# Optimization experiments

Hardware: AMD Instinct MI355X
Metric: run time of the kernel (lower is better)

The kernel has to match this reference:

```python
import jax, jax.numpy as jnp
import numpy as np

P, B, S = 128, 32, 64          # num_packet, batch, bytes per packet
E = 50                          # byte/packet embedding size (hard-coded in module)
Hb = 128; Hp = 128; Po = 128   # byte hidden, packet hidden, packet output
V = 256 * 256; NCLS = 11


def setup_inputs() -> dict:
    key = jax.random.key(0)
    ks = jax.random.split(key, 12)
    rn = lambda k, shp, s: (jax.random.normal(k, shp, jnp.float32) * s)
    return {
        'flow': jax.random.randint(ks[0], (P, B, S), 0, V),
        'emb': rn(ks[1], (V, E), 0.1),
        'byte_Wih': rn(ks[2], (2, 3 * Hb, E), 1.0 / np.sqrt(E)),
        'byte_Whh': rn(ks[3], (2, 3 * Hb, Hb), 1.0 / np.sqrt(Hb)),
        'byte_attn_W': rn(ks[4], (E, 2 * Hb), 1.0 / np.sqrt(2 * Hb)),
        'byte_attn_b': jnp.zeros((E,), jnp.float32),
        'pkt_Wih': rn(ks[5], (2, 3 * Hp, E), 1.0 / np.sqrt(E)),
        'pkt_Whh': rn(ks[6], (2, 3 * Hp, Hp), 1.0 / np.sqrt(Hp)),
        'pkt_attn_W': rn(ks[7], (Po, 2 * Hp), 1.0 / np.sqrt(2 * Hp)),
        'pkt_attn_b': jnp.zeros((Po,), jnp.float32),
        'cls_W': rn(ks[8], (NCLS, Po), 1.0 / np.sqrt(Po)),
        'cls_b': jnp.zeros((NCLS,), jnp.float32),
        'h0_bytes': rn(ks[9], (P, 2, B, Hb), 1.0),   # per-packet random h0 (torch.randn in fwd)
        'h0_packet': rn(ks[10], (2, B, Hp), 1.0),
    }


def _gru_dir(xW, h0, Whh, H):
    # xW: (S, N, 3H) precomputed input projections; h0: (N, H). PyTorch gate order r,z,n; no bias.
    def step(h, xw):
        hW = h @ Whh.T
        r = jax.nn.sigmoid(xw[:, :H] + hW[:, :H])
        z = jax.nn.sigmoid(xw[:, H:2 * H] + hW[:, H:2 * H])
        n = jnp.tanh(xw[:, 2 * H:] + r * hW[:, 2 * H:])
        h_new = (1.0 - z) * n + z * h
        return h_new, h_new
    hT, ys = jax.lax.scan(step, h0, xW)
    return ys, hT


def bigru(x, h0, Wih, Whh, H):
    # x: (S, N, E); h0: (2, N, H) -> outputs (S, N, 2H), final hidden (2, N, H)
    xWf = jnp.einsum('sne,ge->sng', x, Wih[0])
    xWb = jnp.einsum('sne,ge->sng', x[::-1], Wih[1])
    yf, hf = _gru_dir(xWf, h0[0], Whh[0], H)
    yb, hb = _gru_dir(xWb, h0[1], Whh[1], H)
    return jnp.concatenate([yf, yb[::-1]], axis=-1), jnp.stack([hf, hb])


def reference(flow, emb, byte_Wih, byte_Whh, byte_attn_W, byte_attn_b,
              pkt_Wih, pkt_Whh, pkt_attn_W, pkt_attn_b, cls_W, cls_b,
              h0_bytes, h0_packet):
    Pn, Bn, Sn = flow.shape
    x = emb[flow]                                             # (P, B, S, E)
    # Fold packets into batch: one byte-level bi-GRU call instead of a Python loop over P.
    xs = x.transpose(2, 0, 1, 3).reshape(Sn, Pn * Bn, E)      # (S, P*B, E)
    h0b = h0_bytes.transpose(1, 0, 2, 3).reshape(2, Pn * Bn, Hb)
    y, hn = bigru(xs, h0b, byte_Wih, byte_Whh, Hb)            # y (S, P*B, 2Hb), hn (2, P*B, Hb)
    out = y.transpose(1, 0, 2).reshape(Pn, Bn, Sn, 2 * Hb)    # (P, B, S, 2Hb)
    # torch view(-1, 2Hb, 1) on each per-packet (2, B, Hb) final state == raw C-order reshape
    hn_p = hn.reshape(2, Pn, Bn, Hb).transpose(1, 0, 2, 3).reshape(Pn, Bn, 2 * Hb)
    aw = jax.nn.softmax(jnp.einsum('pbsh,pbh->pbs', out, hn_p), axis=-1)
    ctx = jnp.einsum('pbsh,pbs->pbh', out, aw)                # (P, B, 2Hb)
    enc = ctx @ byte_attn_W.T + byte_attn_b                   # (P, B, E)

    y2, hn2 = bigru(enc, h0_packet, pkt_Wih, pkt_Whh, Hp)     # (P, B, 2Hp), (2, B, Hp)
    out2 = y2.transpose(1, 0, 2)                              # (B, P, 2Hp)
    hn2v = hn2.reshape(Bn, 2 * Hp)                            # view(-1, byte_hidden*2) semantics
    aw2 = jax.nn.softmax(jnp.einsum('bph,bh->bp', out2, hn2v), axis=-1)
    ctx2 = jnp.einsum('bph,bp->bh', out2, aw2)                # (B, 2Hp)
    o = ctx2 @ pkt_attn_W.T + pkt_attn_b                      # (B, Po)
    return o @ cls_W.T + cls_b                                # (B, 11)
```

## Files before the change

### kernel.cpp

```cpp
#include <hip/hip_runtime.h>
#include <hip/hip_bf16.h>

#define PD 128
#define BD 32
#define SD 64
#define ED 50
#define HD 128
#define GD 384
#define ND 4096
#define VD 65536
#define LW 128

typedef __attribute__((ext_vector_type(8))) short bf16x8;
typedef __attribute__((ext_vector_type(4))) float f32x4;

__device__ __forceinline__ float sigm(float x) { return 1.0f / (1.0f + __expf(-x)); }
__device__ __forceinline__ float tanh_f(float x) { return 1.0f - 2.0f / (__expf(2.0f * x) + 1.0f); }

__device__ __forceinline__ unsigned short f2b(float f) {
    union { float f; unsigned u; } a; a.f = f;
    unsigned r = a.u + 0x7FFFu + ((a.u >> 16) & 1u);
    return (unsigned short)(r >> 16);
}
__device__ __forceinline__ float b2f(unsigned short h) {
    union { unsigned u; float f; } a; a.u = ((unsigned)h) << 16; return a.f;
}

union frag_u { bf16x8 v; unsigned short s[8]; };

__device__ __forceinline__ void pin_v(bf16x8& v) { asm volatile("" : "+v"(v)); }

#define MFMA(acc, a, b) acc = __builtin_amdgcn_mfma_f32_16x16x32_bf16(a, b, acc, 0, 0, 0)

__device__ __forceinline__ void block_sync_lds() {
    asm volatile("s_waitcnt lgkmcnt(0)" ::: "memory");
    __builtin_amdgcn_sched_barrier(0);
    __builtin_amdgcn_s_barrier();
    __builtin_amdgcn_sched_barrier(0);
}

__global__ void prep_all(const float* __restrict__ emb, unsigned short* __restrict__ embHi,
                         const float* __restrict__ aW, float* __restrict__ aWT,
                         const float* __restrict__ pWih, float* __restrict__ pWT) {
    int idx = blockIdx.x * 256 + threadIdx.x;
    if (idx < VD * 64) {
        int row = idx >> 6, e = idx & 63;
        float v = (e < ED) ? emb[row * ED + e] : 0.f;
        embHi[idx] = f2b(v);
    }
    if (idx < 256 * 64) {
        int c = idx >> 6, e = idx & 63;
        aWT[idx] = (e < ED) ? aW[e * 256 + c] : 0.f;
    }
    if (idx < 2 * 64 * GD) {
        int g = idx % GD, r = idx / GD;
        int d = r >> 6, e = r & 63;
        pWT[idx] = (e < ED) ? pWih[((size_t)(d * GD + g)) * ED + e] : 0.f;
    }
}

__global__ __attribute__((amdgpu_flat_work_group_size(512, 512), amdgpu_waves_per_eu(2, 2)))
void byte_gru_mfma(
    const int* __restrict__ flow, const unsigned short* __restrict__ embHi,
    const float* __restrict__ Wih, const float* __restrict__ Whh,
    const float* __restrict__ h0b,
    unsigned short* __restrict__ y, float* __restrict__ hn) {
    const int dir   = blockIdx.x >> 7;
    const int chunk = blockIdx.x & 127;
    const int n0    = chunk * 32;
    const int tid   = threadIdx.x;
    const int w     = tid >> 6;
    const int lane  = tid & 63;
    const int col   = lane & 15;
    const int kq    = lane >> 4;
    const int u     = w * 16 + col;

    __shared__ unsigned short HHI[2][32 * LW];
    __shared__ unsigned short HLO[2][32 * LW];
    __shared__ int FLOWT[SD * 32];

    const int yrow = tid >> 4;
    const int yu0  = (tid & 15) * 8;
    const int ysw  = yrow * LW + (yu0 ^ ((yrow & 7) << 3));

    bf16x8 WHh[3][4], WHl[3][4], WXh[3][2], WXl[3][2];
    {
        const float* WhhD = Whh + dir * GD * HD;
        #pragma unroll
        for (int g3 = 0; g3 < 3; ++g3) {
            const float* row = WhhD + (g3 * HD + u) * HD;
            #pragma unroll
            for (int kt = 0; kt < 4; ++kt) {
                const int k0 = kt * 32 + kq * 8;
                frag_u h_, l_;
                #pragma unroll
                for (int b = 0; b < 8; ++b) {
                    float v = row[k0 + b];
                    unsigned short hi = f2b(v);
                    h_.s[b] = hi; l_.s[b] = f2b(v - b2f(hi));
                }
                WHh[g3][kt] = h_.v; WHl[g3][kt] = l_.v;
                pin_v(WHh[g3][kt]); pin_v(WHl[g3][kt]);
            }
        }
        const float* WihD = Wih + dir * GD * ED;
        #pragma unroll
        for (int g3 = 0; g3 < 3; ++g3) {
            const float* row = WihD + (g3 * HD + u) * ED;
            #pragma unroll
            for (int kx = 0; kx < 2; ++kx) {
                const int k0 = kx * 32 + kq * 8;
                frag_u h_, l_;
                #pragma unroll
                for (int b = 0; b < 8; ++b) {
                    const int e = k0 + b;
                    float v = (e < ED) ? row[e] : 0.f;
                    unsigned short hi = f2b(v);
                    h_.s[b] = hi; l_.s[b] = f2b(v - b2f(hi));
                }
                WXh[g3][kx] = h_.v; WXl[g3][kx] = l_.v;
                pin_v(WXh[g3][kx]); pin_v(WXl[g3][kx]);
            }
        }
    }

    float hreg[2][4];
    {
        const float* h0row = h0b + (size_t)((chunk * 2 + dir) * 32) * HD;
        #pragma unroll
        for (int m = 0; m < 2; ++m)
            #pragma unroll
            for (int j = 0; j < 4; ++j)
                hreg[m][j] = h0row[(m * 16 + kq * 4 + j) * HD + u];
        for (int idx = tid; idx < 32 * HD; idx += 512) {
            int seq = idx >> 7, uu = idx & 127;
            float v = h0row[idx];
            unsigned short hi = f2b(v);
            int sw = seq * LW + (uu ^ ((seq & 7) << 3));
            HHI[0][sw] = hi; HLO[0][sw] = f2b(v - b2f(hi));
        }
        for (int j = tid; j < SD * 32; j += 512) {
            int s = j >> 5, seq = j & 31;
            FLOWT[j] = flow[(n0 + seq) * SD + s];
        }
    }
    block_sync_lds();

    bf16x8 xa00, xa01, xa10, xa11;
    {
        const int s0 = dir ? (SD - 1) : 0;
        int i0 = FLOWT[s0 * 32 + col];
        int i1 = FLOWT[s0 * 32 + 16 + col];
        const bf16x8* r0 = (const bf16x8*)(embHi + (size_t)i0 * 64);
        const bf16x8* r1 = (const bf16x8*)(embHi + (size_t)i1 * 64);
        xa00 = r0[kq]; xa01 = r0[4 + kq];
        xa10 = r1[kq]; xa11 = r1[4 + kq];
    }

    int par = 0;
    for (int t = 0; t < SD; ++t) {
        const int s = dir ? (SD - 1 - t) : t;

        if (t > 0) {
            const int sp = dir ? (SD - t) : (t - 1);
            uint4 v = *(const uint4*)&HHI[par][ysw];
            *(uint4*)&y[((size_t)(sp * ND) + n0 + yrow) * 256 + dir * HD + yu0] = v;
        }

        bf16x8 xn00, xn01, xn10, xn11;
        if (t < SD - 1) {
            const int sn = dir ? (SD - 2 - t) : (t + 1);
            int i0 = FLOWT[sn * 32 + col];
            int i1 = FLOWT[sn * 32 + 16 + col];
            const bf16x8* r0 = (const bf16x8*)(embHi + (size_t)i0 * 64);
            const bf16x8* r1 = (const bf16x8*)(embHi + (size_t)i1 * 64);
            xn00 = r0[kq]; xn01 = r0[4 + kq];
            xn10 = r1[kq]; xn11 = r1[4 + kq];
        }

        f32x4 aR[2], aZ[2], aHN[2], aXN[2];
        const f32x4 zero = {0.f, 0.f, 0.f, 0.f};
        #pragma unroll
        for (int m = 0; m < 2; ++m) { aR[m] = zero; aZ[m] = zero; aHN[m] = zero; aXN[m] = zero; }

        const unsigned short* HHIp = HHI[par];
        const unsigned short* HLOp = HLO[par];
        #pragma unroll
        for (int kt = 0; kt < 4; ++kt) {
            const int off = kt * 32 + kq * 8;
            const int sw0 = col * LW + (off ^ ((col & 7) << 3));
            const int sw1 = sw0 + 16 * LW;
            bf16x8 ah0 = *(const bf16x8*)&HHIp[sw0];
            bf16x8 al0 = *(const bf16x8*)&HLOp[sw0];
            bf16x8 ah1 = *(const bf16x8*)&HHIp[sw1];
            bf16x8 al1 = *(const bf16x8*)&HLOp[sw1];
            MFMA(aR[0], ah0, WHh[0][kt]); MFMA(aR[0], al0, WHh[0][kt]); MFMA(aR[0], ah0, WHl[0][kt]);
            MFMA(aZ[0], ah0, WHh[1][kt]); MFMA(aZ[0], al0, WHh[1][kt]); MFMA(aZ[0], ah0, WHl[1][kt]);
            MFMA(aHN[0], ah0, WHh[2][kt]); MFMA(aHN[0], al0, WHh[2][kt]); MFMA(aHN[0], ah0, WHl[2][kt]);
            MFMA(aR[1], ah1, WHh[0][kt]); MFMA(aR[1], al1, WHh[0][kt]); MFMA(aR[1], ah1, WHl[0][kt]);
            MFMA(aZ[1], ah1, WHh[1][kt]); MFMA(aZ[1], al1, WHh[1][kt]); MFMA(aZ[1], ah1, WHl[1][kt]);
            MFMA(aHN[1], ah1, WHh[2][kt]); MFMA(aHN[1], al1, WHh[2][kt]); MFMA(aHN[1], ah1, WHl[2][kt]);
        }
        #pragma unroll
        for (int kx = 0; kx < 2; ++kx) {
            bf16x8 x0 = kx ? xa01 : xa00;
            bf16x8 x1 = kx ? xa11 : xa10;
            MFMA(aR[0], x0, WXh[0][kx]); MFMA(aR[0], x0, WXl[0][kx]);
            MFMA(aZ[0], x0, WXh[1][kx]); MFMA(aZ[0], x0, WXl[1][kx]);
            MFMA(aXN[0], x0, WXh[2][kx]); MFMA(aXN[0], x0, WXl[2][kx]);
            MFMA(aR[1], x1, WXh[0][kx]); MFMA(aR[1], x1, WXl[0][kx]);
            MFMA(aZ[1], x1, WXh[1][kx]); MFMA(aZ[1], x1, WXl[1][kx]);
            MFMA(aXN[1], x1, WXh[2][kx]); MFMA(aXN[1], x1, WXl[2][kx]);
        }

        unsigned short* HHIn = HHI[par ^ 1];
        unsigned short* HLOn = HLO[par ^ 1];
        #pragma unroll
        for (int m = 0; m < 2; ++m)
            #pragma unroll
            for (int j = 0; j < 4; ++j) {
                float r = sigm(aR[m][j]);
                float z = sigm(aZ[m][j]);
                float nn = tanh_f(aXN[m][j] + r * aHN[m][j]);
                float hnew = (1.f - z) * nn + z * hreg[m][j];
                hreg[m][j] = hnew;
                __hip_bfloat16 bh = __float2bfloat16(hnew);
                unsigned short hi = *(unsigned short*)&bh;
                __hip_bfloat16 bl = __float2bfloat16(hnew - b2f(hi));
                const int seq = m * 16 + kq * 4 + j;
                const int sw = seq * LW + (u ^ ((seq & 7) << 3));
                HHIn[sw] = hi;
                HLOn[sw] = *(unsigned short*)&bl;
            }
        block_sync_lds();
        xa00 = xn00; xa01 = xn01; xa10 = xn10; xa11 = xn11;
        par ^= 1;
    }
    {
        const int sl = dir ? 0 : (SD - 1);
        uint4 v = *(const uint4*)&HHI[par][ysw];
        *(uint4*)&y[((size_t)(sl * ND) + n0 + yrow) * 256 + dir * HD + yu0] = v;
    }
    #pragma unroll
    for (int m = 0; m < 2; ++m)
        #pragma unroll
        for (int j = 0; j < 4; ++j) {
            int seq = m * 16 + kq * 4 + j;
            hn[((size_t)dir * ND + n0 + seq) * HD + u] = hreg[m][j];
        }
}

__global__ __launch_bounds__(256) void byte_attn(
    const unsigned short* __restrict__ y, const float* __restrict__ hn,
    const float* __restrict__ aWT, const float* __restrict__ ab,
    const float* __restrict__ pWT, float* __restrict__ pxw) {
    const int n = blockIdx.x;
    const int p = n >> 5, irow = n & 31;
    const int tid = threadIdx.x;
    __shared__ unsigned short yl[SD][256];
    __shared__ float hnl[256];
    __shared__ float red[256];
    __shared__ float awl[SD];
    __shared__ float ctxl[256];
    __shared__ float encl[64];

    for (int idx = tid; idx < SD * 32; idx += 256) {
        int s = idx >> 5, cc = (idx & 31) * 8;
        *(uint4*)&yl[s][cc] = *(const uint4*)&y[((s * ND) + n) * 256 + cc];
    }
    {
        int c = tid;
        int idx = irow * 256 + c;
        int d = idx >> 12, bb = (idx >> 7) & 31, uu = idx & 127;
        hnl[c] = hn[(d * ND + p * 32 + bb) * HD + uu];
    }
    __syncthreads();
    {
        int s = tid & 63, grp = tid >> 6;
        float acc = 0.f;
        for (int k = 0; k < 32; ++k) {
            int c2 = grp * 32 + ((s + k) & 31);
            unsigned pair = *(const unsigned*)&yl[s][c2 * 2];
            float2 hv = *(const float2*)&hnl[c2 * 2];
            union { unsigned u; float f; } lo, hi;
            lo.u = pair << 16; hi.u = pair & 0xFFFF0000u;
            acc += lo.f * hv.x + hi.f * hv.y;
        }
        red[grp * 64 + s] = acc;
    }
    __syncthreads();
    if (tid < 64) {
        float sc = red[tid] + red[64 + tid] + red[128 + tid] + red[192 + tid];
        float m = sc;
        #pragma unroll
        for (int o = 32; o; o >>= 1) m = fmaxf(m, __shfl_xor(m, o));
        float e = __expf(sc - m);
        float ssum = e;
        #pragma unroll
        for (int o = 32; o; o >>= 1) ssum += __shfl_xor(ssum, o);
        awl[tid] = e / ssum;
    }
    __syncthreads();
    {
        int c = tid;
        float acc = 0.f;
        for (int s = 0; s < SD; ++s) acc += awl[s] * b2f(yl[s][c]);
        ctxl[c] = acc;
    }
    __syncthreads();
    {
        int e = tid & 63, q = tid >> 6;
        float acc = 0.f;
        for (int c = q * 64; c < q * 64 + 64; ++c) acc += ctxl[c] * aWT[c * 64 + e];
        red[q * 64 + e] = acc;
    }
    __syncthreads();
    if (tid < 64) {
        float v = red[tid] + red[64 + tid] + red[128 + tid] + red[192 + tid];
        encl[tid] = (tid < ED) ? (v + ab[tid]) : 0.f;
    }
    __syncthreads();
    #pragma unroll
    for (int k = 0; k < 3; ++k) {
        int fg = tid + k * 256;
        int d = fg >= GD, g = fg - d * GD;
        const float* wr = pWT + (size_t)(d * 64) * GD + g;
        float acc = 0.f;
        #pragma unroll 2
        for (int e = 0; e < ED; ++e) acc += encl[e] * wr[(size_t)e * GD];
        pxw[((size_t)(d * PD + p) * 32 + irow) * GD + g] = acc;
    }
}

__global__ __launch_bounds__(384, 1) void pkt_gru(
    const float* __restrict__ pxw, const float* __restrict__ Whh,
    const float* __restrict__ h0p,
    float* __restrict__ y2, float* __restrict__ hn2) {
    const int d = blockIdx.x >> 5, sq = blockIdx.x & 31;
    const int tid = threadIdx.x;
    __shared__ float hcur[HD];
    __shared__ float hw[GD];
    float w[HD];
    const float* wrow = Whh + (d * GD + tid) * HD;
    #pragma unroll
    for (int k = 0; k < HD; ++k) w[k] = wrow[k];
    if (tid < HD) hcur[tid] = h0p[(d * 32 + sq) * HD + tid];

    float xr = 0.f, xz = 0.f, xn_ = 0.f;
    if (tid < HD) {
        const int p0 = d ? (PD - 1) : 0;
        const float* xw = pxw + (size_t)((d * PD + p0) * 32 + sq) * GD;
        xr = xw[tid]; xz = xw[HD + tid]; xn_ = xw[2 * HD + tid];
    }
    block_sync_lds();
    for (int t = 0; t < PD; ++t) {
        const int pp = d ? (PD - 1 - t) : t;
        float xrn = 0.f, xzn = 0.f, xnn = 0.f;
        if (t < PD - 1 && tid < HD) {
            const int pn = d ? (PD - 2 - t) : (t + 1);
            const float* xw = pxw + (size_t)((d * PD + pn) * 32 + sq) * GD;
            xrn = xw[tid]; xzn = xw[HD + tid]; xnn = xw[2 * HD + tid];
        }
        float a0 = 0.f, a1 = 0.f, a2 = 0.f, a3 = 0.f;
        #pragma unroll
        for (int kc = 0; kc < 32; ++kc) {
            float4 h4 = *(const float4*)&hcur[kc * 4];
            a0 += w[4 * kc + 0] * h4.x; a1 += w[4 * kc + 1] * h4.y;
            a2 += w[4 * kc + 2] * h4.z; a3 += w[4 * kc + 3] * h4.w;
        }
        hw[tid] = (a0 + a1) + (a2 + a3);
        block_sync_lds();
        if (tid < HD) {
            int uu = tid;
            float r = sigm(xr + hw[uu]);
            float z = sigm(xz + hw[HD + uu]);
            float nn = tanh_f(xn_ + r * hw[2 * HD + uu]);
            float hnew = (1.f - z) * nn + z * hcur[uu];
            hcur[uu] = hnew;
            y2[(pp * 32 + sq) * 256 + d * HD + uu] = hnew;
        }
        block_sync_lds();
        xr = xrn; xz = xzn; xn_ = xnn;
    }
    if (tid < HD) hn2[(d * 32 + sq) * HD + tid] = hcur[tid];
}

__global__ __launch_bounds__(256) void pkt_attn_cls(
    const float* __restrict__ y2, const float* __restrict__ hn2,
    const float* __restrict__ aW, const float* __restrict__ ab,
    const float* __restrict__ cW, const float* __restrict__ cb,
    float* __restrict__ out) {
    const int b = blockIdx.x;
    const int tid = threadIdx.x;
    __shared__ float yl2[32][257];
    __shared__ float hnl[256];
    __shared__ float red[256];
    __shared__ float scl[PD];
    __shared__ float awl[PD];
    __shared__ float ctxl[256];
    __shared__ float ol[HD];
    hnl[tid] = hn2[(((b >> 4) * 32) + 2 * (b & 15) + (tid >> 7)) * HD + (tid & 127)];
    for (int ch = 0; ch < 4; ++ch) {
        __syncthreads();
        for (int idx = tid; idx < 32 * 256; idx += 256) {
            int r = idx >> 8, c = idx & 255;
            yl2[r][c] = y2[((ch * 32 + r) * 32 + b) * 256 + c];
        }
        __syncthreads();
        {
            int r = tid >> 3, seg = tid & 7;
            float acc = 0.f;
            for (int i = 0; i < 32; ++i) {
                int c = seg * 32 + ((i + seg * 4) & 31);
                acc += yl2[r][c] * hnl[c];
            }
            red[tid] = acc;
        }
        __syncthreads();
        if (tid < 32) {
            float s = 0.f;
            #pragma unroll
            for (int k = 0; k < 8; ++k) s += red[tid * 8 + k];
            scl[ch * 32 + tid] = s;
        }
    }
    __syncthreads();
    if (tid < 64) {
        float s0 = scl[tid], s1 = scl[64 + tid];
        float m = fmaxf(s0, s1);
        #pragma unroll
        for (int o = 32; o; o >>= 1) m = fmaxf(m, __shfl_xor(m, o));
        float e0 = __expf(s0 - m), e1 = __expf(s1 - m);
        float ss = e0 + e1;
        #pragma unroll
        for (int o = 32; o; o >>= 1) ss += __shfl_xor(ss, o);
        awl[tid] = e0 / ss; awl[64 + tid] = e1 / ss;
    }
    __syncthreads();
    {
        int c = tid;
        float acc = 0.f;
        for (int p2 = 0; p2 < PD; ++p2) acc += awl[p2] * y2[(p2 * 32 + b) * 256 + c];
        ctxl[c] = acc;
    }
    __syncthreads();
    {
        int h = tid >> 1, hf = tid & 1;
        const float* wr = aW + h * 256 + hf * 128;
        const float* cr = ctxl + hf * 128;
        float acc = 0.f;
        for (int c = 0; c < 128; ++c) acc += cr[c] * wr[c];
        red[hf * 128 + h] = acc;
    }
    __syncthreads();
    if (tid < HD) ol[tid] = red[tid] + red[128 + tid] + ab[tid];
    __syncthreads();
    if (tid < 11) {
        float acc = cb[tid];
        for (int h = 0; h < HD; ++h) acc += ol[h] * cW[tid * HD + h];
        out[b * 11 + tid] = acc;
    }
}

extern "C" void kernel_launch(void* const* d_in, const int* in_sizes, int n_in,
                              void* d_out, int out_size, void* d_ws, size_t ws_size,
                              hipStream_t stream) {
    const int*   flow = (const int*)d_in[0];
    const float* emb  = (const float*)d_in[1];
    const float* bWih = (const float*)d_in[2];
    const float* bWhh = (const float*)d_in[3];
    const float* baW  = (const float*)d_in[4];
    const float* bab  = (const float*)d_in[5];
    const float* pWih = (const float*)d_in[6];
    const float* pWhh = (const float*)d_in[7];
    const float* paW  = (const float*)d_in[8];
    const float* pab  = (const float*)d_in[9];
    const float* cW   = (const float*)d_in[10];
    const float* cb   = (const float*)d_in[11];
    const float* h0b  = (const float*)d_in[12];
    const float* h0p  = (const float*)d_in[13];
    float* out = (float*)d_out;

    char* ws = (char*)d_ws;
    size_t off = 0;
    unsigned short* y = (unsigned short*)(ws + off); off += (size_t)SD * ND * 256 * 2;
    float* hn    = (float*)(ws + off); off += (size_t)2 * ND * HD * 4;
    float* pxw   = (float*)(ws + off); off += (size_t)2 * PD * 32 * GD * 4;
    float* y2    = (float*)(ws + off); off += (size_t)PD * 32 * 256 * 4;
    float* hn2   = (float*)(ws + off); off += (size_t)2 * 32 * HD * 4;
    unsigned short* embHi = (unsigned short*)(ws + off); off += (size_t)VD * 64 * 2;
    float* aWT   = (float*)(ws + off); off += (size_t)256 * 64 * 4;
    float* pWT   = (float*)(ws + off); off += (size_t)2 * 64 * GD * 4;
    if (ws_size < off) return;

    prep_all<<<(VD * 64 + 255) / 256, 256, 0, stream>>>(emb, embHi, baW, aWT, pWih, pWT);
    byte_gru_mfma<<<256, 512, 0, stream>>>(flow, embHi, bWih, bWhh, h0b, y, hn);
    byte_attn<<<ND, 256, 0, stream>>>(y, hn, aWT, bab, pWT, pxw);
    pkt_gru<<<64, 384, 0, stream>>>(pxw, pWhh, h0p, y2, hn2);
    pkt_attn_cls<<<32, 256, 0, stream>>>(y2, hn2, paW, pab, cW, cb, out);
}
```

Baseline: 532.2 us.

## Pre-transpose and pre-swizzle weights in prep kernel for coalesced loads

```diff
diff --git a/kernel.cpp b/kernel.cpp
--- a/kernel.cpp
+++ b/kernel.cpp
@@ -41,7 +41,11 @@
 
 __global__ void prep_all(const float* __restrict__ emb, unsigned short* __restrict__ embHi,
                          const float* __restrict__ aW, float* __restrict__ aWT,
-                         const float* __restrict__ pWih, float* __restrict__ pWT) {
+                         const float* __restrict__ pWih, float* __restrict__ pWT,
+                         const float* __restrict__ pWhh, float* __restrict__ pWhhT,
+                         const float* __restrict__ paW, float* __restrict__ paWT,
+                         const float* __restrict__ bWhh, float* __restrict__ bWhhS,
+                         const float* __restrict__ bWih, float* __restrict__ bWihS) {
     int idx = blockIdx.x * 256 + threadIdx.x;
     if (idx < VD * 64) {
         int row = idx >> 6, e = idx & 63;
@@ -57,12 +61,36 @@
         int d = r >> 6, e = r & 63;
         pWT[idx] = (e < ED) ? pWih[((size_t)(d * GD + g)) * ED + e] : 0.f;
     }
+    if (idx < 2 * HD * GD) {
+        int g = idx % GD, r = idx / GD;
+        int d = r >> 7, k = r & 127;
+        pWhhT[idx] = pWhh[((size_t)(d * GD + g)) * HD + k];
+    }
+    if (idx < 256 * HD) {
+        int c = idx >> 7, h = idx & 127;
+        paWT[idx] = paW[h * 256 + c];
+    }
+    if (idx < 2 * 3 * 4 * 512 * 8) {
+        int b = idx & 7, t = (idx >> 3) & 511;
+        int kt = (idx >> 12) & 3, r3 = idx >> 14;
+        int g3 = r3 % 3, dir = r3 / 3;
+        int u = ((t >> 6) * 16) + (t & 15), kq = (t >> 4) & 3;
+        bWhhS[idx] = bWhh[((size_t)(dir * GD + g3 * HD + u)) * HD + kt * 32 + kq * 8 + b];
+    }
+    if (idx < 2 * 3 * 2 * 512 * 8) {
+        int b = idx & 7, t = (idx >> 3) & 511;
+        int kx = (idx >> 12) & 1, r3 = idx >> 13;
+        int g3 = r3 % 3, dir = r3 / 3;
+        int u = ((t >> 6) * 16) + (t & 15), kq = (t >> 4) & 3;
+        int e = kx * 32 + kq * 8 + b;
+        bWihS[idx] = (e < ED) ? bWih[((size_t)(dir * GD + g3 * HD + u)) * ED + e] : 0.f;
+    }
 }
 
 __global__ __attribute__((amdgpu_flat_work_group_size(512, 512), amdgpu_waves_per_eu(2, 2)))
 void byte_gru_mfma(
     const int* __restrict__ flow, const unsigned short* __restrict__ embHi,
-    const float* __restrict__ Wih, const float* __restrict__ Whh,
+    const float* __restrict__ bWihS, const float* __restrict__ bWhhS,
     const float* __restrict__ h0b,
     unsigned short* __restrict__ y, float* __restrict__ hn) {
     const int dir   = blockIdx.x >> 7;
@@ -85,43 +113,40 @@
 
     bf16x8 WHh[3][4], WHl[3][4], WXh[3][2], WXl[3][2];
     {
-        const float* WhhD = Whh + dir * GD * HD;
-        #pragma unroll
-        for (int g3 = 0; g3 < 3; ++g3) {
-            const float* row = WhhD + (g3 * HD + u) * HD;
+        #pragma unroll
+        for (int g3 = 0; g3 < 3; ++g3)
             #pragma unroll
             for (int kt = 0; kt < 4; ++kt) {
-                const int k0 = kt * 32 + kq * 8;
+                const float* src = bWhhS + (((size_t)((dir * 3 + g3) * 4 + kt)) * 512 + tid) * 8;
+                float4 v0 = *(const float4*)src;
+                float4 v1 = *(const float4*)(src + 4);
+                float vals[8] = {v0.x, v0.y, v0.z, v0.w, v1.x, v1.y, v1.z, v1.w};
                 frag_u h_, l_;
                 #pragma unroll
                 for (int b = 0; b < 8; ++b) {
-                    float v = row[k0 + b];
-                    unsigned short hi = f2b(v);
-                    h_.s[b] = hi; l_.s[b] = f2b(v - b2f(hi));
+                    unsigned short hi = f2b(vals[b]);
+                    h_.s[b] = hi; l_.s[b] = f2b(vals[b] - b2f(hi));
                 }
                 WHh[g3][kt] = h_.v; WHl[g3][kt] = l_.v;
                 pin_v(WHh[g3][kt]); pin_v(WHl[g3][kt]);
             }
-        }
-        const float* WihD = Wih + dir * GD * ED;
-        #pragma unroll
-        for (int g3 = 0; g3 < 3; ++g3) {
-            const float* row = WihD + (g3 * HD + u) * ED;
+        #pragma unroll
+        for (int g3 = 0; g3 < 3; ++g3)
             #pragma unroll
             for (int kx = 0; kx < 2; ++kx) {
-                const int k0 = kx * 32 + kq * 8;
+                const float* src = bWihS + (((size_t)((dir * 3 + g3) * 2 + kx)) * 512 + tid) * 8;
+                float4 v0 = *(const float4*)src;
+                float4 v1 = *(const float4*)(src + 4);
+                float vals[8] = {v0.x, v0.y, v0.z, v0.w, v1.x, v1.y, v1.z, v1.w};
                 frag_u h_, l_;
                 #pragma unroll
                 for (int b = 0; b < 8; ++b) {
-                    const int e = k0 + b;
-                    float v = (e < ED) ? row[e] : 0.f;
-                    unsigned short hi = f2b(v);
-                    h_.s[b] = hi; l_.s[b] = f2b(v - b2f(hi));
+                    unsigned short hi = f2b(vals[b]);
+                    h_.s[b] = hi; l_.s[b] = f2b(vals[b] - b2f(hi));
                 }
                 WXh[g3][kx] = h_.v; WXl[g3][kx] = l_.v;
                 pin_v(WXh[g3][kx]); pin_v(WXl[g3][kx]);
             }
-        }
     }
 
     float hreg[2][4];
@@ -333,7 +358,7 @@
 }
 
 __global__ __launch_bounds__(384, 1) void pkt_gru(
-    const float* __restrict__ pxw, const float* __restrict__ Whh,
+    const float* __restrict__ pxw, const float* __restrict__ pWhhT,
     const float* __restrict__ h0p,
     float* __restrict__ y2, float* __restrict__ hn2) {
     const int d = blockIdx.x >> 5, sq = blockIdx.x & 31;
@@ -341,9 +366,8 @@
     __shared__ float hcur[HD];
     __shared__ float hw[GD];
     float w[HD];
-    const float* wrow = Whh + (d * GD + tid) * HD;
     #pragma unroll
-    for (int k = 0; k < HD; ++k) w[k] = wrow[k];
+    for (int k = 0; k < HD; ++k) w[k] = pWhhT[((size_t)(d * HD + k)) * GD + tid];
     if (tid < HD) hcur[tid] = h0p[(d * 32 + sq) * HD + tid];
 
     float xr = 0.f, xz = 0.f, xn_ = 0.f;
@@ -387,7 +411,7 @@
 
 __global__ __launch_bounds__(256) void pkt_attn_cls(
     const float* __restrict__ y2, const float* __restrict__ hn2,
-    const float* __restrict__ aW, const float* __restrict__ ab,
+    const float* __restrict__ paWT, const float* __restrict__ ab,
     const float* __restrict__ cW, const float* __restrict__ cb,
     float* __restrict__ out) {
     const int b = blockIdx.x;
@@ -445,11 +469,9 @@
     }
     __syncthreads();
     {
-        int h = tid >> 1, hf = tid & 1;
-        const float* wr = aW + h * 256 + hf * 128;
-        const float* cr = ctxl + hf * 128;
+        int h = tid & 127, hf = tid >> 7;
         float acc = 0.f;
-        for (int c = 0; c < 128; ++c) acc += cr[c] * wr[c];
+        for (int c = hf * 128; c < hf * 128 + 128; ++c) acc += ctxl[c] * paWT[c * 128 + h];
         red[hf * 128 + h] = acc;
     }
     __syncthreads();
@@ -491,11 +513,16 @@
     unsigned short* embHi = (unsigned short*)(ws + off); off += (size_t)VD * 64 * 2;
     float* aWT   = (float*)(ws + off); off += (size_t)256 * 64 * 4;
     float* pWT   = (float*)(ws + off); off += (size_t)2 * 64 * GD * 4;
+    float* pWhhT = (float*)(ws + off); off += (size_t)2 * HD * GD * 4;
+    float* paWT  = (float*)(ws + off); off += (size_t)256 * HD * 4;
+    float* bWhhS = (float*)(ws + off); off += (size_t)2 * 3 * 4 * 512 * 8 * 4;
+    float* bWihS = (float*)(ws + off); off += (size_t)2 * 3 * 2 * 512 * 8 * 4;
     if (ws_size < off) return;
 
-    prep_all<<<(VD * 64 + 255) / 256, 256, 0, stream>>>(emb, embHi, baW, aWT, pWih, pWT);
-    byte_gru_mfma<<<256, 512, 0, stream>>>(flow, embHi, bWih, bWhh, h0b, y, hn);
+    prep_all<<<(VD * 64 + 255) / 256, 256, 0, stream>>>(
+        emb, embHi, baW, aWT, pWih, pWT, pWhh, pWhhT, paW, paWT, bWhh, bWhhS, bWih, bWihS);
+    byte_gru_mfma<<<256, 512, 0, stream>>>(flow, embHi, bWihS, bWhhS, h0b, y, hn);
     byte_attn<<<ND, 256, 0, stream>>>(y, hn, aWT, bab, pWT, pxw);
-    pkt_gru<<<64, 384, 0, stream>>>(pxw, pWhh, h0p, y2, hn2);
-    pkt_attn_cls<<<32, 256, 0, stream>>>(y2, hn2, paW, pab, cW, cb, out);
-}
+    pkt_gru<<<64, 384, 0, stream>>>(pxw, pWhhT, h0p, y2, hn2);
+    pkt_attn_cls<<<32, 256, 0, stream>>>(y2, hn2, paWT, pab, cW, cb, out);
+}
```

Measured after the change: 561.2 us. 1.05x slower.
